# Kernel optimization log

Measured on AMD Instinct MI355X. Metric: run time of the kernel, lower is better.

Reference implementation:

```python
import jax, jax.numpy as jnp
import numpy as np

N, DIN, C, E = 50000, 256, 8, 1600000
N_STEPS = 5


def setup_inputs() -> dict:
    key = jax.random.key(0)
    k1, k2, k3, k4 = jax.random.split(key, 4)
    x = jax.random.normal(k1, (N, DIN), dtype=jnp.float32)
    W = jax.random.normal(k2, (DIN, C), dtype=jnp.float32) / np.float32(np.sqrt(DIN))
    b = jnp.zeros((C,), dtype=jnp.float32)
    edge_index = jax.random.randint(k3, (2, E), 0, N, dtype=jnp.int64)
    rv = jax.random.randint(k4, (E,), 0, E, dtype=jnp.int64)
    return {"x": x, "W": W, "b": b, "edge_index": edge_index, "rv": rv}


def _log_normalize(lx):
    return lx - jax.scipy.special.logsumexp(lx, axis=-1, keepdims=True)


def reference(x, W, b, edge_index, rv):
    # transform: Linear (num_hidden=0) + LogSoftmax -> initial log beliefs
    log_b0 = jax.nn.log_softmax(x @ W + b, axis=-1)            # [N, C]
    src, dst = edge_index[0], edge_index[1]
    n_nodes, n_cls = log_b0.shape
    # learn_coupling=False: log_H = -3 * (ones - eye)
    logH = -3.0 * (jnp.ones((n_cls, n_cls), jnp.float32) - jnp.eye(n_cls, dtype=jnp.float32))
    log_msg = jnp.full((edge_index.shape[1], n_cls), -np.log(n_cls), dtype=jnp.float32)
    log_b = log_b0
    for _ in range(N_STEPS):
        x_j = log_b[src]                                        # [E, C] gather
        t = x_j - log_msg[rv]                                   # [E, C]
        # per-edge logsumexp over incoming class dim against coupling matrix
        raw = jax.scipy.special.logsumexp(t[:, :, None] + logH[None, :, :], axis=1)  # [E, C]
        log_msg = _log_normalize(raw)
        agg = jax.ops.segment_sum(log_msg, dst, num_segments=n_nodes)  # scatter-add
        log_b = _log_normalize(agg + log_b0)
    return log_b
```

## Files before the change

kernel.cpp:

```cpp
#include <hip/hip_runtime.h>

static constexpr int kN   = 50000;
static constexpr int kDin = 256;
static constexpr int kC   = 8;
static constexpr int kE   = 1600000;
static constexpr int kSteps = 5;

static constexpr int kNB        = 256;
static constexpr int kBucketW   = 196;
static constexpr int kChunk     = 4096;

static constexpr size_t OFF_LOGB0 = 0;
static constexpr size_t OFF_BHIST = 1600000;
static constexpr size_t OFF_GBASE = 1601024;
static constexpr size_t OFF_GCUR  = 1602112;
static constexpr size_t OFF_START = 1603200;
static constexpr size_t OFF_REC   = 1803264;
static constexpr size_t OFF_INV   = 8203264;
static constexpr size_t OFF_MSGA  = 14603264;
static constexpr size_t OFF_MSGB  = 40203264;
static constexpr size_t WS_NEEDED = 65803264;

static constexpr float kDEC   = 3.0f / 65535.0f;
static constexpr float kENC   = 65535.0f / 3.0f;
static constexpr float kOFF   = 3.2990003f;
static constexpr float kA     = 0.049787068367863944f;
static constexpr float kOneMA = 0.950212931632136f;

__global__ void __launch_bounds__(256) phase1_kernel(
    const float* __restrict__ x, const float* __restrict__ W,
    const float* __restrict__ bias,
    float* __restrict__ log_b0, float* __restrict__ log_b)
{
    const int lane   = threadIdx.x & 63;
    const int wave   = (blockIdx.x * blockDim.x + threadIdx.x) >> 6;
    const int nwaves = (gridDim.x * blockDim.x) >> 6;

    float w[4][8];
#pragma unroll
    for (int j = 0; j < 4; ++j) {
        const float4* wp = reinterpret_cast<const float4*>(W + (size_t)(lane + 64 * j) * kC);
        float4 a = wp[0], b2 = wp[1];
        w[j][0] = a.x;  w[j][1] = a.y;  w[j][2] = a.z;  w[j][3] = a.w;
        w[j][4] = b2.x; w[j][5] = b2.y; w[j][6] = b2.z; w[j][7] = b2.w;
    }

    for (int row = wave; row < kN; row += nwaves) {
        const float* xr = x + (size_t)row * kDin;
        float acc[8] = {0.f, 0.f, 0.f, 0.f, 0.f, 0.f, 0.f, 0.f};
#pragma unroll
        for (int j = 0; j < 4; ++j) {
            float xv = xr[lane + 64 * j];
#pragma unroll
            for (int c = 0; c < 8; ++c) acc[c] = fmaf(xv, w[j][c], acc[c]);
        }
#pragma unroll
        for (int off = 32; off > 0; off >>= 1) {
#pragma unroll
            for (int c = 0; c < 8; ++c) acc[c] += __shfl_down(acc[c], off, 64);
        }
        if (lane == 0) {
            float z[8], m = -1e30f;
#pragma unroll
            for (int c = 0; c < 8; ++c) { z[c] = acc[c] + bias[c]; m = fmaxf(m, z[c]); }
            float s = 0.f;
#pragma unroll
            for (int c = 0; c < 8; ++c) s += __expf(z[c] - m);
            float lse = m + __logf(s);
#pragma unroll
            for (int c = 0; c < 8; ++c) {
                float v = z[c] - lse;
                log_b0[(size_t)row * 8 + c] = v;
                log_b[(size_t)row * 8 + c]  = v;
            }
        }
    }
}

__global__ void __launch_bounds__(256) bucket_hist_kernel(
    const int* __restrict__ dst, int* __restrict__ bhist)
{
    __shared__ int h[kNB];
    h[threadIdx.x] = 0;
    __syncthreads();
    for (int e = blockIdx.x * blockDim.x + threadIdx.x; e < kE;
         e += gridDim.x * blockDim.x)
        atomicAdd(&h[dst[e] / kBucketW], 1);
    __syncthreads();
    if (h[threadIdx.x]) atomicAdd(&bhist[threadIdx.x], h[threadIdx.x]);
}

__global__ void __launch_bounds__(256) bucket_scan_kernel(
    const int* __restrict__ bhist, int* __restrict__ gbase, int* __restrict__ gcur)
{
    __shared__ int sh[kNB];
    const int tid = threadIdx.x;
    int v = bhist[tid];
    sh[tid] = v;
    __syncthreads();
#pragma unroll
    for (int off = 1; off < kNB; off <<= 1) {
        int t = (tid >= off) ? sh[tid - off] : 0;
        __syncthreads();
        sh[tid] += t;
        __syncthreads();
    }
    int excl = sh[tid] - v;
    gbase[tid] = excl;
    gcur[tid]  = excl;
    if (tid == kNB - 1) { gbase[kNB] = sh[tid]; gcur[kNB] = sh[tid]; }
}

__global__ void __launch_bounds__(256) bin_kernel(
    const int* __restrict__ dst, int* __restrict__ gcur,
    unsigned int* __restrict__ recbuf)
{
    __shared__ int hist[kNB];
    __shared__ int sh[kNB];
    __shared__ int cursor[kNB];
    __shared__ unsigned int buf[kChunk];

    const int tid = threadIdx.x;
    const int e0  = blockIdx.x * kChunk;
    const int n   = (kE - e0 < kChunk) ? (kE - e0) : kChunk;

    hist[tid] = 0;
    __syncthreads();

    int myb[16];
    unsigned int rec[16];
#pragma unroll
    for (int k = 0; k < 16; ++k) {
        const int i = tid + k * 256;
        myb[k] = -1;
        if (i < n) {
            const int d = dst[e0 + i];
            const int b = d / kBucketW;
            myb[k] = b;
            rec[k] = ((unsigned int)(d - b * kBucketW) << 21) | (unsigned int)(e0 + i);
            atomicAdd(&hist[b], 1);
        }
    }
    __syncthreads();

    const int cnt = hist[tid];
    sh[tid] = cnt;
    __syncthreads();
#pragma unroll
    for (int off = 1; off < kNB; off <<= 1) {
        int t = (tid >= off) ? sh[tid - off] : 0;
        __syncthreads();
        sh[tid] += t;
        __syncthreads();
    }
    const int excl = sh[tid] - cnt;
    cursor[tid] = excl;
    __syncthreads();

#pragma unroll
    for (int k = 0; k < 16; ++k) {
        if (myb[k] >= 0) {
            int slot = atomicAdd(&cursor[myb[k]], 1);
            buf[slot] = rec[k];
        }
    }
    __syncthreads();

    if (cnt > 0) {
        int gd = atomicAdd(&gcur[tid], cnt);
        for (int q = 0; q < cnt; ++q)
            recbuf[gd + q] = buf[excl + q];
    }
}

__global__ void __launch_bounds__(256) fine_kernel(
    const int* __restrict__ gbase, const unsigned int* __restrict__ recbuf,
    int* __restrict__ start, int* __restrict__ inv)
{
    __shared__ int hist[kNB];
    __shared__ int sh[kNB];
    __shared__ int lcur[kNB];

    const int tid = threadIdx.x;
    const int b   = blockIdx.x;
    const int nb0 = b * kBucketW;
    const int nnode = (kN - nb0 < kBucketW) ? (kN - nb0) : kBucketW;
    const int rb = gbase[b], re = gbase[b + 1];

    hist[tid] = 0;
    __syncthreads();

    for (int i = rb + tid; i < re; i += 256)
        atomicAdd(&hist[recbuf[i] >> 21], 1);
    __syncthreads();

    const int cnt = hist[tid];
    sh[tid] = cnt;
    __syncthreads();
#pragma unroll
    for (int off = 1; off < kNB; off <<= 1) {
        int t = (tid >= off) ? sh[tid - off] : 0;
        __syncthreads();
        sh[tid] += t;
        __syncthreads();
    }
    const int excl = sh[tid] - cnt;
    lcur[tid] = rb + excl;
    if (tid < nnode) start[nb0 + tid] = rb + excl;
    if (b == gridDim.x - 1 && tid == 0) start[kN] = kE;
    __syncthreads();

    for (int i = rb + tid; i < re; i += 256) {
        const unsigned int r = recbuf[i];
        const int p = atomicAdd(&lcur[r >> 21], 1);
        inv[p] = (int)(r & 0x1FFFFFu);
    }
}

template <bool FIRST>
__global__ void __launch_bounds__(256) edge_kernel(
    const int* __restrict__ src, const int* __restrict__ rv,
    const float* __restrict__ log_b,
    const unsigned short* __restrict__ mold,
    unsigned short* __restrict__ mnew)
{
    const int e = blockIdx.x * blockDim.x + threadIdx.x;
    if (e >= kE) return;
    const int s = src[e];

    float t[8];
    {
        const float4* lb = reinterpret_cast<const float4*>(log_b + (size_t)s * 8);
        float4 a = lb[0], b2 = lb[1];
        t[0] = a.x;  t[1] = a.y;  t[2] = a.z;  t[3] = a.w;
        t[4] = b2.x; t[5] = b2.y; t[6] = b2.z; t[7] = b2.w;
    }
    if (!FIRST) {
        const int r = rv[e];
        uint4 m = *reinterpret_cast<const uint4*>(mold + (size_t)r * 8);
        t[0] -= (float)(m.x & 0xffffu) * kDEC;
        t[1] -= (float)(m.x >> 16)     * kDEC;
        t[2] -= (float)(m.y & 0xffffu) * kDEC;
        t[3] -= (float)(m.y >> 16)     * kDEC;
        t[4] -= (float)(m.z & 0xffffu) * kDEC;
        t[5] -= (float)(m.z >> 16)     * kDEC;
        t[6] -= (float)(m.w & 0xffffu) * kDEC;
        t[7] -= (float)(m.w >> 16)     * kDEC;
    }

    float mx = t[0];
#pragma unroll
    for (int c = 1; c < 8; ++c) mx = fmaxf(mx, t[c]);
    float p[8], S = 0.f;
#pragma unroll
    for (int c = 0; c < 8; ++c) { p[c] = __expf(t[c] - mx); S += p[c]; }

    const float coef = kOneMA / S;
    unsigned int q[8];
#pragma unroll
    for (int c = 0; c < 8; ++c) {
        float u  = fmaf(coef, p[c], kA);
        float qq = fmaf(__logf(u), kENC, 65535.0f);
        qq = fminf(fmaxf(qq + 0.5f, 0.0f), 65535.0f);
        q[c] = (unsigned int)qq;
    }
    uint4 outv = make_uint4(q[0] | (q[1] << 16), q[2] | (q[3] << 16),
                            q[4] | (q[5] << 16), q[6] | (q[7] << 16));
    *reinterpret_cast<uint4*>(mnew + (size_t)e * 8) = outv;
}

__global__ void __launch_bounds__(256) node_kernel(
    const int* __restrict__ start, const int* __restrict__ inv,
    const unsigned short* __restrict__ msgq,
    const float* __restrict__ log_b0, float* __restrict__ log_b)
{
    const int gtid = blockIdx.x * blockDim.x + threadIdx.x;
    const int n = gtid >> 6;
    if (n >= kN) return;
    const int lane = threadIdx.x & 63;
    const int sub = lane >> 3, c = lane & 7;
    const int s = start[n], e2 = start[n + 1];

    int Q = 0;
    for (int j = s + sub; j < e2; j += 8)
        Q += (int)msgq[(size_t)inv[j] * 8 + c];
    Q += __shfl_xor(Q, 8, 64);
    Q += __shfl_xor(Q, 16, 64);
    Q += __shfl_xor(Q, 32, 64);

    const int deg = e2 - s;
    float v = fmaf((float)Q, kDEC, -kOFF * (float)deg) + log_b0[(size_t)n * 8 + c];

    float m = v;
    m = fmaxf(m, __shfl_xor(m, 1, 64));
    m = fmaxf(m, __shfl_xor(m, 2, 64));
    m = fmaxf(m, __shfl_xor(m, 4, 64));
    float sum = __expf(v - m);
    sum += __shfl_xor(sum, 1, 64);
    sum += __shfl_xor(sum, 2, 64);
    sum += __shfl_xor(sum, 4, 64);
    float lse = m + __logf(sum);

    if (sub == 0) log_b[(size_t)n * 8 + c] = v - lse;
}

extern "C" void kernel_launch(void* const* d_in, const int* in_sizes, int n_in,
                              void* d_out, int out_size, void* d_ws, size_t ws_size,
                              hipStream_t stream) {
    const float* x    = (const float*)d_in[0];
    const float* W    = (const float*)d_in[1];
    const float* bias = (const float*)d_in[2];
    const int*   ei   = (const int*)d_in[3];
    const int*   rv   = (const int*)d_in[4];
    const int* src = ei;
    const int* dst = ei + kE;
    float* out = (float*)d_out;

    if (ws_size < WS_NEEDED) return;

    char* ws = (char*)d_ws;
    float* log_b0 = (float*)(ws + OFF_LOGB0);
    int*   bhist  = (int*)(ws + OFF_BHIST);
    int*   gbase  = (int*)(ws + OFF_GBASE);
    int*   gcur   = (int*)(ws + OFF_GCUR);
    int*   start  = (int*)(ws + OFF_START);
    unsigned int* recbuf = (unsigned int*)(ws + OFF_REC);
    int*   inv    = (int*)(ws + OFF_INV);
    unsigned short* msgA = (unsigned short*)(ws + OFF_MSGA);
    unsigned short* msgB = (unsigned short*)(ws + OFF_MSGB);

    const int edgeBlocks = (kE + 255) / 256;
    const int nodeBlocks = (kN * 64 + 255) / 256;
    const int binBlocks  = (kE + kChunk - 1) / kChunk;

    (void)hipMemsetAsync(bhist, 0, kNB * sizeof(int), stream);
    phase1_kernel<<<1024, 256, 0, stream>>>(x, W, bias, log_b0, out);

    bucket_hist_kernel<<<256, 256, 0, stream>>>(dst, bhist);
    bucket_scan_kernel<<<1, 256, 0, stream>>>(bhist, gbase, gcur);
    bin_kernel<<<binBlocks, 256, 0, stream>>>(dst, gcur, recbuf);
    fine_kernel<<<kNB, 256, 0, stream>>>(gbase, recbuf, start, inv);

    edge_kernel<true><<<edgeBlocks, 256, 0, stream>>>(src, rv, out, msgB, msgA);
    node_kernel<<<nodeBlocks, 256, 0, stream>>>(start, inv, msgA, log_b0, out);

    unsigned short* cur = msgA;
    unsigned short* nxt = msgB;
    for (int it = 1; it < kSteps; ++it) {
        edge_kernel<false><<<edgeBlocks, 256, 0, stream>>>(src, rv, out, cur, nxt);
        node_kernel<<<nodeBlocks, 256, 0, stream>>>(start, inv, nxt, log_b0, out);
        unsigned short* tmp = cur; cur = nxt; nxt = tmp;
    }
}
```

Baseline: 503.1 us.

## Fuse init with histogram, widen edge/node kernels, skip intermediate belief normalization

Merges the linear+log-softmax init and the destination bucket histogram into a single launch by giving extra blocks the histogram job. bin_kernel now copies binned records to global memory with all threads in parallel, using a binary search over the bucket prefix sums, instead of a per-bucket serial loop. The edge kernel handles two edges per thread with paired index loads. The node kernel gives each node a half-wave that reads whole 16-byte packed messages, replacing per-class 2-byte loads. The per-step log-normalization of beliefs is skipped except on the final step, which relies on the next edge softmax being shift-invariant; the cost is larger unnormalized magnitudes in intermediate beliefs.

```diff
diff --git a/kernel.cpp b/kernel.cpp
--- a/kernel.cpp
+++ b/kernel.cpp
@@ -27,14 +27,27 @@
 static constexpr float kA     = 0.049787068367863944f;
 static constexpr float kOneMA = 0.950212931632136f;
 
-__global__ void __launch_bounds__(256) phase1_kernel(
+__global__ void __launch_bounds__(256) init_kernel(
     const float* __restrict__ x, const float* __restrict__ W,
     const float* __restrict__ bias,
-    float* __restrict__ log_b0, float* __restrict__ log_b)
-{
+    float* __restrict__ log_b0, float* __restrict__ log_b,
+    const int* __restrict__ dst, int* __restrict__ bhist)
+{
+    __shared__ int h[kNB];
+    if (blockIdx.x >= 1024) {
+        h[threadIdx.x] = 0;
+        __syncthreads();
+        const int nthr = 256 * 256;
+        for (int e = (blockIdx.x - 1024) * 256 + threadIdx.x; e < kE; e += nthr)
+            atomicAdd(&h[dst[e] / kBucketW], 1);
+        __syncthreads();
+        if (h[threadIdx.x]) atomicAdd(&bhist[threadIdx.x], h[threadIdx.x]);
+        return;
+    }
+
     const int lane   = threadIdx.x & 63;
-    const int wave   = (blockIdx.x * blockDim.x + threadIdx.x) >> 6;
-    const int nwaves = (gridDim.x * blockDim.x) >> 6;
+    const int wave   = (blockIdx.x * 256 + threadIdx.x) >> 6;
+    const int nwaves = (1024 * 256) >> 6;
 
     float w[4][8];
 #pragma unroll
@@ -77,19 +90,6 @@
     }
 }
 
-__global__ void __launch_bounds__(256) bucket_hist_kernel(
-    const int* __restrict__ dst, int* __restrict__ bhist)
-{
-    __shared__ int h[kNB];
-    h[threadIdx.x] = 0;
-    __syncthreads();
-    for (int e = blockIdx.x * blockDim.x + threadIdx.x; e < kE;
-         e += gridDim.x * blockDim.x)
-        atomicAdd(&h[dst[e] / kBucketW], 1);
-    __syncthreads();
-    if (h[threadIdx.x]) atomicAdd(&bhist[threadIdx.x], h[threadIdx.x]);
-}
-
 __global__ void __launch_bounds__(256) bucket_scan_kernel(
     const int* __restrict__ bhist, int* __restrict__ gbase, int* __restrict__ gcur)
 {
@@ -118,6 +118,7 @@
     __shared__ int hist[kNB];
     __shared__ int sh[kNB];
     __shared__ int cursor[kNB];
+    __shared__ int gdbase[kNB];
     __shared__ unsigned int buf[kChunk];
 
     const int tid = threadIdx.x;
@@ -164,12 +165,16 @@
             buf[slot] = rec[k];
         }
     }
-    __syncthreads();
-
-    if (cnt > 0) {
-        int gd = atomicAdd(&gcur[tid], cnt);
-        for (int q = 0; q < cnt; ++q)
-            recbuf[gd + q] = buf[excl + q];
+    gdbase[tid] = (cnt > 0) ? atomicAdd(&gcur[tid], cnt) : 0;
+    __syncthreads();
+
+    for (int i = tid; i < n; i += 256) {
+        int b = 0;
+#pragma unroll
+        for (int step = 128; step >= 1; step >>= 1)
+            if (b + step <= kNB - 1 && sh[b + step - 1] <= i) b += step;
+        const int off_in_b = i - (sh[b] - hist[b]);
+        recbuf[gdbase[b] + off_in_b] = buf[i];
     }
 }
 
@@ -224,84 +229,135 @@
     const unsigned short* __restrict__ mold,
     unsigned short* __restrict__ mnew)
 {
-    const int e = blockIdx.x * blockDim.x + threadIdx.x;
-    if (e >= kE) return;
-    const int s = src[e];
-
-    float t[8];
+    const int e0 = (blockIdx.x * 256 + threadIdx.x) * 2;
+    if (e0 >= kE) return;
+
+    const int2 sp = *reinterpret_cast<const int2*>(src + e0);
+
+    const float4* lba = reinterpret_cast<const float4*>(log_b + (size_t)sp.x * 8);
+    const float4* lbb = reinterpret_cast<const float4*>(log_b + (size_t)sp.y * 8);
+    float4 a0 = lba[0], a1 = lba[1];
+    float4 b0 = lbb[0], b1 = lbb[1];
+
+    uint4 ma, mb;
+    if (!FIRST) {
+        const int2 rp = *reinterpret_cast<const int2*>(rv + e0);
+        ma = *reinterpret_cast<const uint4*>(mold + (size_t)rp.x * 8);
+        mb = *reinterpret_cast<const uint4*>(mold + (size_t)rp.y * 8);
+    }
+
+    float ta[8] = {a0.x, a0.y, a0.z, a0.w, a1.x, a1.y, a1.z, a1.w};
+    float tb[8] = {b0.x, b0.y, b0.z, b0.w, b1.x, b1.y, b1.z, b1.w};
+    if (!FIRST) {
+        ta[0] -= (float)(ma.x & 0xffffu) * kDEC;  ta[1] -= (float)(ma.x >> 16) * kDEC;
+        ta[2] -= (float)(ma.y & 0xffffu) * kDEC;  ta[3] -= (float)(ma.y >> 16) * kDEC;
+        ta[4] -= (float)(ma.z & 0xffffu) * kDEC;  ta[5] -= (float)(ma.z >> 16) * kDEC;
+        ta[6] -= (float)(ma.w & 0xffffu) * kDEC;  ta[7] -= (float)(ma.w >> 16) * kDEC;
+        tb[0] -= (float)(mb.x & 0xffffu) * kDEC;  tb[1] -= (float)(mb.x >> 16) * kDEC;
+        tb[2] -= (float)(mb.y & 0xffffu) * kDEC;  tb[3] -= (float)(mb.y >> 16) * kDEC;
+        tb[4] -= (float)(mb.z & 0xffffu) * kDEC;  tb[5] -= (float)(mb.z >> 16) * kDEC;
+        tb[6] -= (float)(mb.w & 0xffffu) * kDEC;  tb[7] -= (float)(mb.w >> 16) * kDEC;
+    }
+
+    unsigned int qa[8], qb[8];
     {
-        const float4* lb = reinterpret_cast<const float4*>(log_b + (size_t)s * 8);
-        float4 a = lb[0], b2 = lb[1];
-        t[0] = a.x;  t[1] = a.y;  t[2] = a.z;  t[3] = a.w;
-        t[4] = b2.x; t[5] = b2.y; t[6] = b2.z; t[7] = b2.w;
-    }
-    if (!FIRST) {
-        const int r = rv[e];
-        uint4 m = *reinterpret_cast<const uint4*>(mold + (size_t)r * 8);
-        t[0] -= (float)(m.x & 0xffffu) * kDEC;
-        t[1] -= (float)(m.x >> 16)     * kDEC;
-        t[2] -= (float)(m.y & 0xffffu) * kDEC;
-        t[3] -= (float)(m.y >> 16)     * kDEC;
-        t[4] -= (float)(m.z & 0xffffu) * kDEC;
-        t[5] -= (float)(m.z >> 16)     * kDEC;
-        t[6] -= (float)(m.w & 0xffffu) * kDEC;
-        t[7] -= (float)(m.w >> 16)     * kDEC;
-    }
-
-    float mx = t[0];
-#pragma unroll
-    for (int c = 1; c < 8; ++c) mx = fmaxf(mx, t[c]);
-    float p[8], S = 0.f;
-#pragma unroll
-    for (int c = 0; c < 8; ++c) { p[c] = __expf(t[c] - mx); S += p[c]; }
-
-    const float coef = kOneMA / S;
-    unsigned int q[8];
-#pragma unroll
-    for (int c = 0; c < 8; ++c) {
-        float u  = fmaf(coef, p[c], kA);
-        float qq = fmaf(__logf(u), kENC, 65535.0f);
-        qq = fminf(fmaxf(qq + 0.5f, 0.0f), 65535.0f);
-        q[c] = (unsigned int)qq;
-    }
-    uint4 outv = make_uint4(q[0] | (q[1] << 16), q[2] | (q[3] << 16),
-                            q[4] | (q[5] << 16), q[6] | (q[7] << 16));
-    *reinterpret_cast<uint4*>(mnew + (size_t)e * 8) = outv;
-}
-
+        float mx = ta[0];
+#pragma unroll
+        for (int c = 1; c < 8; ++c) mx = fmaxf(mx, ta[c]);
+        float p[8], S = 0.f;
+#pragma unroll
+        for (int c = 0; c < 8; ++c) { p[c] = __expf(ta[c] - mx); S += p[c]; }
+        const float coef = kOneMA / S;
+#pragma unroll
+        for (int c = 0; c < 8; ++c) {
+            float u  = fmaf(coef, p[c], kA);
+            float qq = fmaf(__logf(u), kENC, 65535.0f);
+            qq = fminf(fmaxf(qq + 0.5f, 0.0f), 65535.0f);
+            qa[c] = (unsigned int)qq;
+        }
+    }
+    {
+        float mx = tb[0];
+#pragma unroll
+        for (int c = 1; c < 8; ++c) mx = fmaxf(mx, tb[c]);
+        float p[8], S = 0.f;
+#pragma unroll
+        for (int c = 0; c < 8; ++c) { p[c] = __expf(tb[c] - mx); S += p[c]; }
+        const float coef = kOneMA / S;
+#pragma unroll
+        for (int c = 0; c < 8; ++c) {
+            float u  = fmaf(coef, p[c], kA);
+            float qq = fmaf(__logf(u), kENC, 65535.0f);
+            qq = fminf(fmaxf(qq + 0.5f, 0.0f), 65535.0f);
+            qb[c] = (unsigned int)qq;
+        }
+    }
+
+    uint4* mn = reinterpret_cast<uint4*>(mnew + (size_t)e0 * 8);
+    mn[0] = make_uint4(qa[0] | (qa[1] << 16), qa[2] | (qa[3] << 16),
+                       qa[4] | (qa[5] << 16), qa[6] | (qa[7] << 16));
+    mn[1] = make_uint4(qb[0] | (qb[1] << 16), qb[2] | (qb[3] << 16),
+                       qb[4] | (qb[5] << 16), qb[6] | (qb[7] << 16));
+}
+
+template <bool FINAL>
 __global__ void __launch_bounds__(256) node_kernel(
     const int* __restrict__ start, const int* __restrict__ inv,
     const unsigned short* __restrict__ msgq,
     const float* __restrict__ log_b0, float* __restrict__ log_b)
 {
-    const int gtid = blockIdx.x * blockDim.x + threadIdx.x;
-    const int n = gtid >> 6;
+    const int wid  = (blockIdx.x * 256 + threadIdx.x) >> 6;
+    const int lane = threadIdx.x & 63;
+    const int half = lane >> 5;
+    const int l32  = lane & 31;
+    const int n = wid * 2 + half;
     if (n >= kN) return;
-    const int lane = threadIdx.x & 63;
-    const int sub = lane >> 3, c = lane & 7;
+
     const int s = start[n], e2 = start[n + 1];
 
-    int Q = 0;
-    for (int j = s + sub; j < e2; j += 8)
-        Q += (int)msgq[(size_t)inv[j] * 8 + c];
-    Q += __shfl_xor(Q, 8, 64);
-    Q += __shfl_xor(Q, 16, 64);
-    Q += __shfl_xor(Q, 32, 64);
-
-    const int deg = e2 - s;
-    float v = fmaf((float)Q, kDEC, -kOFF * (float)deg) + log_b0[(size_t)n * 8 + c];
-
-    float m = v;
-    m = fmaxf(m, __shfl_xor(m, 1, 64));
-    m = fmaxf(m, __shfl_xor(m, 2, 64));
-    m = fmaxf(m, __shfl_xor(m, 4, 64));
-    float sum = __expf(v - m);
-    sum += __shfl_xor(sum, 1, 64);
-    sum += __shfl_xor(sum, 2, 64);
-    sum += __shfl_xor(sum, 4, 64);
-    float lse = m + __logf(sum);
-
-    if (sub == 0) log_b[(size_t)n * 8 + c] = v - lse;
+    int q[8] = {0, 0, 0, 0, 0, 0, 0, 0};
+    for (int j = s + l32; j < e2; j += 32) {
+        const uint4 m = *reinterpret_cast<const uint4*>(msgq + (size_t)inv[j] * 8);
+        q[0] += (int)(m.x & 0xffffu);  q[1] += (int)(m.x >> 16);
+        q[2] += (int)(m.y & 0xffffu);  q[3] += (int)(m.y >> 16);
+        q[4] += (int)(m.z & 0xffffu);  q[5] += (int)(m.z >> 16);
+        q[6] += (int)(m.w & 0xffffu);  q[7] += (int)(m.w >> 16);
+    }
+#pragma unroll
+    for (int off = 1; off <= 16; off <<= 1) {
+#pragma unroll
+        for (int c = 0; c < 8; ++c) q[c] += __shfl_xor(q[c], off, 64);
+    }
+
+    if (l32 == 0) {
+        const int deg = e2 - s;
+        const float base = -kOFF * (float)deg;
+        const float4* lb0 = reinterpret_cast<const float4*>(log_b0 + (size_t)n * 8);
+        float4 c0 = lb0[0], c1 = lb0[1];
+        float v[8];
+        v[0] = fmaf((float)q[0], kDEC, base) + c0.x;
+        v[1] = fmaf((float)q[1], kDEC, base) + c0.y;
+        v[2] = fmaf((float)q[2], kDEC, base) + c0.z;
+        v[3] = fmaf((float)q[3], kDEC, base) + c0.w;
+        v[4] = fmaf((float)q[4], kDEC, base) + c1.x;
+        v[5] = fmaf((float)q[5], kDEC, base) + c1.y;
+        v[6] = fmaf((float)q[6], kDEC, base) + c1.z;
+        v[7] = fmaf((float)q[7], kDEC, base) + c1.w;
+        if (FINAL) {
+            float m = v[0];
+#pragma unroll
+            for (int c = 1; c < 8; ++c) m = fmaxf(m, v[c]);
+            float sum = 0.f;
+#pragma unroll
+            for (int c = 0; c < 8; ++c) sum += __expf(v[c] - m);
+            float lse = m + __logf(sum);
+#pragma unroll
+            for (int c = 0; c < 8; ++c) v[c] -= lse;
+        }
+        float4* lb = reinterpret_cast<float4*>(log_b + (size_t)n * 8);
+        lb[0] = make_float4(v[0], v[1], v[2], v[3]);
+        lb[1] = make_float4(v[4], v[5], v[6], v[7]);
+    }
 }
 
 extern "C" void kernel_launch(void* const* d_in, const int* in_sizes, int n_in,
@@ -329,26 +385,27 @@
     unsigned short* msgA = (unsigned short*)(ws + OFF_MSGA);
     unsigned short* msgB = (unsigned short*)(ws + OFF_MSGB);
 
-    const int edgeBlocks = (kE + 255) / 256;
-    const int nodeBlocks = (kN * 64 + 255) / 256;
+    const int edgeBlocks = (kE / 2 + 255) / 256;
+    const int nodeBlocks = ((kN + 1) / 2 * 64 + 255) / 256;
     const int binBlocks  = (kE + kChunk - 1) / kChunk;
 
     (void)hipMemsetAsync(bhist, 0, kNB * sizeof(int), stream);
-    phase1_kernel<<<1024, 256, 0, stream>>>(x, W, bias, log_b0, out);
-
-    bucket_hist_kernel<<<256, 256, 0, stream>>>(dst, bhist);
+    init_kernel<<<1280, 256, 0, stream>>>(x, W, bias, log_b0, out, dst, bhist);
     bucket_scan_kernel<<<1, 256, 0, stream>>>(bhist, gbase, gcur);
     bin_kernel<<<binBlocks, 256, 0, stream>>>(dst, gcur, recbuf);
     fine_kernel<<<kNB, 256, 0, stream>>>(gbase, recbuf, start, inv);
 
     edge_kernel<true><<<edgeBlocks, 256, 0, stream>>>(src, rv, out, msgB, msgA);
-    node_kernel<<<nodeBlocks, 256, 0, stream>>>(start, inv, msgA, log_b0, out);
+    node_kernel<false><<<nodeBlocks, 256, 0, stream>>>(start, inv, msgA, log_b0, out);
 
     unsigned short* cur = msgA;
     unsigned short* nxt = msgB;
     for (int it = 1; it < kSteps; ++it) {
         edge_kernel<false><<<edgeBlocks, 256, 0, stream>>>(src, rv, out, cur, nxt);
-        node_kernel<<<nodeBlocks, 256, 0, stream>>>(start, inv, nxt, log_b0, out);
+        if (it == kSteps - 1)
+            node_kernel<true><<<nodeBlocks, 256, 0, stream>>>(start, inv, nxt, log_b0, out);
+        else
+            node_kernel<false><<<nodeBlocks, 256, 0, stream>>>(start, inv, nxt, log_b0, out);
         unsigned short* tmp = cur; cur = nxt; nxt = tmp;
     }
 }
```

After: 480.6 us. 1.05x faster.
